# Kernel tuning notes

Hardware: AMD Instinct MI355X
Metric: run time of the kernel (lower is better)

Reference implementation:

```python
import jax, jax.numpy as jnp
import numpy as np

N = 50000      # nodes
E = 800000     # edges (avg degree 16)
IN = 256       # in_feat
OUT = 256      # out_feat
R = 8          # num_rels
B = 4          # num_bases
EPS = 1e-5
NEG_SLOPE = 0.1


def setup_inputs() -> dict:
    key = jax.random.key(0)
    ks = jax.random.split(key, 10)
    node_feats = jax.random.normal(ks[0], (N, IN), dtype=jnp.float32)
    src = jax.random.randint(ks[1], (E,), 0, N, dtype=jnp.int32)
    dst = jax.random.randint(ks[2], (E,), 0, N, dtype=jnp.int32)
    edge_types = jax.random.randint(ks[3], (E,), 0, R, dtype=jnp.int32)
    # RGCN basis-decomposition parameters
    bases = jax.random.normal(ks[4], (B, IN, OUT), dtype=jnp.float32) * (1.0 / np.sqrt(IN))
    comp = jax.random.normal(ks[5], (R, B), dtype=jnp.float32) * (1.0 / np.sqrt(B))
    loop_weight = jax.random.normal(ks[6], (IN, OUT), dtype=jnp.float32) * (1.0 / np.sqrt(IN))
    bias = jnp.zeros((OUT,), dtype=jnp.float32)
    gamma = jnp.ones((OUT,), dtype=jnp.float32)
    beta = jnp.zeros((OUT,), dtype=jnp.float32)
    return {"node_feats": node_feats, "src": src, "dst": dst, "edge_types": edge_types,
            "bases": bases, "comp": comp, "loop_weight": loop_weight, "bias": bias,
            "gamma": gamma, "beta": beta}


def reference(node_feats, src, dst, edge_types, bases, comp, loop_weight, bias, gamma, beta):
    # Basis decomposition: W_r = sum_b comp[r,b] * V_b  -> [R, IN, OUT]
    W = jnp.einsum('rb,bio->rio', comp, bases)
    # Transform all node features under every relation once (avoids per-edge [E,IN,OUT] gather)
    transformed = jnp.einsum('ni,rio->rno', node_feats, W)   # [R, N, OUT]
    msg = transformed[edge_types, src]                        # [E, OUT] gather per edge
    agg = jax.ops.segment_sum(msg, dst, num_segments=N)      # scatter-add to destinations
    # DGL RelGraphConv defaults: self-loop transform + bias
    h = agg + node_feats @ loop_weight + bias                 # [N, OUT]
    # LeakyReLU(0.1)
    h = jnp.where(h > 0, h, NEG_SLOPE * h)
    # LayerNorm over feature dim
    mu = jnp.mean(h, axis=-1, keepdims=True)
    var = jnp.mean(jnp.square(h - mu), axis=-1, keepdims=True)
    return gamma * (h - mu) * jax.lax.rsqrt(var + EPS) + beta
```

## Files before the change

kernel.cpp:

```cpp
#include <hip/hip_runtime.h>

#define NN 50000
#define MP 50048
#define EE 800000
#define RCOLS 2304

typedef __attribute__((ext_vector_type(8))) short short8;
typedef __attribute__((ext_vector_type(4))) float f32x4;

__device__ __forceinline__ float bf2f(unsigned short u) {
  unsigned int x = ((unsigned int)u) << 16;
  float f; __builtin_memcpy(&f, &x, 4); return f;
}
__device__ __forceinline__ unsigned short f2bf(float f) {
  unsigned int x; __builtin_memcpy(&x, &f, 4);
  return (unsigned short)((x + 0x7fffu + ((x >> 16) & 1u)) >> 16);
}

constexpr size_t OFF_XB   = 0;
constexpr size_t OFF_WT   = 25624576;
constexpr size_t OFF_T    = 26804224;
constexpr size_t OFF_CNT  = 257425408;
constexpr size_t OFF_OFFS = 257625408;
constexpr size_t OFF_CUR  = 257825412;
constexpr size_t OFF_EIX  = 258025412;

__global__ __launch_bounds__(256) void build_w_kernel(
    const float* __restrict__ bases, const float* __restrict__ comp,
    const float* __restrict__ loopw, unsigned short* __restrict__ WT) {
  int idx = blockIdx.x * 256 + threadIdx.x;
  if (idx >= RCOLS * 256) return;
  int ogl = idx >> 8;
  int i   = idx & 255;
  float v;
  if (ogl < 2048) {
    int r = ogl >> 8, o = ogl & 255;
    v = 0.f;
#pragma unroll
    for (int b = 0; b < 4; ++b)
      v += comp[r * 4 + b] * bases[((size_t)b * 256 + i) * 256 + o];
  } else {
    v = loopw[i * 256 + (ogl & 255)];
  }
  WT[idx] = f2bf(v);
}

__global__ __launch_bounds__(256) void convert_x_kernel(
    const float* __restrict__ X, unsigned short* __restrict__ Xb) {
  size_t e0 = ((size_t)blockIdx.x * 256 + threadIdx.x) * 4;
  if (e0 >= (size_t)MP * 256) return;
  float4 v = make_float4(0.f, 0.f, 0.f, 0.f);
  if (e0 < (size_t)NN * 256) v = *(const float4*)(X + e0);
  ushort4 o;
  o.x = f2bf(v.x); o.y = f2bf(v.y); o.z = f2bf(v.z); o.w = f2bf(v.w);
  *(ushort4*)(Xb + e0) = o;
}

__global__ __launch_bounds__(256) void gemm_kernel(
    const unsigned short* __restrict__ A,
    const unsigned short* __restrict__ Bt,
    unsigned short* __restrict__ C) {
  __shared__ __align__(16) unsigned short As[128 * 64];
  __shared__ __align__(16) unsigned short Bs[128 * 64];
  const int tid  = threadIdx.x;
  const int lane = tid & 63;
  const int wave = tid >> 6;
  const int wm = wave >> 1, wn = wave & 1;
  const int m0 = blockIdx.x * 128;
  const int n0 = blockIdx.y * 128;

  f32x4 acc[4][4] = {};

  const int srow = tid >> 3;
  const int ke   = (tid & 7) * 8;
  const unsigned int ldsbase = (unsigned int)((tid & ~63) * 16);

  for (int k0 = 0; k0 < 256; k0 += 64) {
#pragma unroll
    for (int p = 0; p < 4; ++p) {
      int row = p * 32 + srow;
      const unsigned short* ga = A  + (size_t)(m0 + row) * 256 + k0 + ke;
      const unsigned short* gb = Bt + (size_t)(n0 + row) * 256 + k0 + ke;
      unsigned int lo = p * 4096 + ldsbase;
      __builtin_amdgcn_global_load_lds(
          (const __attribute__((address_space(1))) unsigned int*)ga,
          (__attribute__((address_space(3))) unsigned int*)((char*)As + lo), 16, 0, 0);
      __builtin_amdgcn_global_load_lds(
          (const __attribute__((address_space(1))) unsigned int*)gb,
          (__attribute__((address_space(3))) unsigned int*)((char*)Bs + lo), 16, 0, 0);
    }
    __syncthreads();

    const int rfr = lane & 15;
    const int kgr = (lane >> 4) * 8;
#pragma unroll
    for (int kk = 0; kk < 2; ++kk) {
      short8 af[4], bfr[4];
#pragma unroll
      for (int m = 0; m < 4; ++m)
        af[m] = *(const short8*)&As[(wm * 64 + m * 16 + rfr) * 64 + kk * 32 + kgr];
#pragma unroll
      for (int n = 0; n < 4; ++n)
        bfr[n] = *(const short8*)&Bs[(wn * 64 + n * 16 + rfr) * 64 + kk * 32 + kgr];
#pragma unroll
      for (int m = 0; m < 4; ++m)
#pragma unroll
        for (int n = 0; n < 4; ++n)
          acc[m][n] = __builtin_amdgcn_mfma_f32_16x16x32_bf16(af[m], bfr[n], acc[m][n], 0, 0, 0);
    }
    __syncthreads();
  }

  const int orow = (lane >> 4) * 4;
  const int ocol = lane & 15;
#pragma unroll
  for (int m = 0; m < 4; ++m)
#pragma unroll
    for (int n = 0; n < 4; ++n) {
      int gr = m0 + wm * 64 + m * 16 + orow;
      int gc = n0 + wn * 64 + n * 16 + ocol;
      unsigned short* cp = C + (size_t)gr * RCOLS + gc;
#pragma unroll
      for (int j = 0; j < 4; ++j)
        cp[(size_t)j * RCOLS] = f2bf(acc[m][n][j]);
    }
}

__global__ __launch_bounds__(256) void count_kernel(const int* __restrict__ dst,
                                                    int* __restrict__ counts) {
  int e = blockIdx.x * 256 + threadIdx.x;
  if (e < EE) atomicAdd(&counts[dst[e]], 1);
}

__global__ __launch_bounds__(1024) void scan_kernel(const int* __restrict__ counts,
                                                    int* __restrict__ offsets) {
  __shared__ int wsum[16];
  __shared__ int carry_s;
  int tid = threadIdx.x, lane = tid & 63, wid = tid >> 6;
  if (tid == 0) carry_s = 0;
  __syncthreads();
  for (int base = 0; base < NN; base += 1024) {
    int i = base + tid;
    int v = (i < NN) ? counts[i] : 0;
    int incl = v;
#pragma unroll
    for (int d = 1; d < 64; d <<= 1) {
      int t = __shfl_up(incl, d, 64);
      if (lane >= d) incl += t;
    }
    if (lane == 63) wsum[wid] = incl;
    __syncthreads();
    int wpre = 0;
    for (int w = 0; w < wid; ++w) wpre += wsum[w];
    if (i < NN) offsets[i] = carry_s + wpre + incl - v;
    __syncthreads();
    if (tid == 1023) carry_s += wpre + incl;
    __syncthreads();
  }
  if (threadIdx.x == 0) offsets[NN] = carry_s;
}

__global__ __launch_bounds__(256) void scatter_kernel(
    const int* __restrict__ src, const int* __restrict__ dst,
    const int* __restrict__ etype, const int* __restrict__ offsets,
    int* __restrict__ cursor, unsigned int* __restrict__ eoff) {
  int e = blockIdx.x * 256 + threadIdx.x;
  if (e < EE) {
    int d = dst[e];
    int pos = atomicAdd(&cursor[d], 1);
    eoff[offsets[d] + pos] = (unsigned int)(src[e] * RCOLS + etype[e] * 256);
  }
}

__global__ __launch_bounds__(256) void finalize_kernel(
    const unsigned short* __restrict__ T, const int* __restrict__ offsets,
    const unsigned int* __restrict__ eoff,
    const float* __restrict__ bias, const float* __restrict__ gamma,
    const float* __restrict__ beta, float* __restrict__ out) {
  int wid = threadIdx.x >> 6, lane = threadIdx.x & 63;
  int n = blockIdx.x * 4 + wid;
  int o4 = lane * 4;
  float a0 = 0.f, a1 = 0.f, a2 = 0.f, a3 = 0.f;
  int s = offsets[n], e = offsets[n + 1];
  for (int i = s; i < e; ++i) {
    ushort4 v = *(const ushort4*)(T + (size_t)eoff[i] + o4);
    a0 += bf2f(v.x); a1 += bf2f(v.y); a2 += bf2f(v.z); a3 += bf2f(v.w);
  }
  ushort4 sl = *(const ushort4*)(T + (size_t)n * RCOLS + 2048 + o4);
  float4 bi = *(const float4*)(bias + o4);
  a0 += bf2f(sl.x) + bi.x; a1 += bf2f(sl.y) + bi.y;
  a2 += bf2f(sl.z) + bi.z; a3 += bf2f(sl.w) + bi.w;
  a0 = a0 > 0.f ? a0 : 0.1f * a0;
  a1 = a1 > 0.f ? a1 : 0.1f * a1;
  a2 = a2 > 0.f ? a2 : 0.1f * a2;
  a3 = a3 > 0.f ? a3 : 0.1f * a3;
  float sum = a0 + a1 + a2 + a3;
  float sq  = a0 * a0 + a1 * a1 + a2 * a2 + a3 * a3;
#pragma unroll
  for (int m = 32; m >= 1; m >>= 1) {
    sum += __shfl_xor(sum, m);
    sq  += __shfl_xor(sq, m);
  }
  float mu  = sum * (1.f / 256.f);
  float var = sq * (1.f / 256.f) - mu * mu;
  float inv = rsqrtf(var + 1e-5f);
  float4 g = *(const float4*)(gamma + o4);
  float4 be = *(const float4*)(beta + o4);
  float4 o;
  o.x = g.x * (a0 - mu) * inv + be.x;
  o.y = g.y * (a1 - mu) * inv + be.y;
  o.z = g.z * (a2 - mu) * inv + be.z;
  o.w = g.w * (a3 - mu) * inv + be.w;
  *(float4*)(out + (size_t)n * 256 + o4) = o;
}

extern "C" void kernel_launch(void* const* d_in, const int* in_sizes, int n_in,
                              void* d_out, int out_size, void* d_ws, size_t ws_size,
                              hipStream_t stream) {
  const float* node_feats = (const float*)d_in[0];
  const int*   src        = (const int*)d_in[1];
  const int*   dst        = (const int*)d_in[2];
  const int*   etype      = (const int*)d_in[3];
  const float* bases      = (const float*)d_in[4];
  const float* comp       = (const float*)d_in[5];
  const float* loopw      = (const float*)d_in[6];
  const float* bias       = (const float*)d_in[7];
  const float* gamma      = (const float*)d_in[8];
  const float* beta       = (const float*)d_in[9];
  float* out = (float*)d_out;

  char* ws = (char*)d_ws;
  unsigned short* Xb   = (unsigned short*)(ws + OFF_XB);
  unsigned short* WT   = (unsigned short*)(ws + OFF_WT);
  unsigned short* T    = (unsigned short*)(ws + OFF_T);
  int*            cnts = (int*)(ws + OFF_CNT);
  int*            offs = (int*)(ws + OFF_OFFS);
  int*            cur  = (int*)(ws + OFF_CUR);
  unsigned int*   eoff = (unsigned int*)(ws + OFF_EIX);

  build_w_kernel<<<(RCOLS * 256 + 255) / 256, 256, 0, stream>>>(bases, comp, loopw, WT);
  convert_x_kernel<<<((MP * 256 / 4) + 255) / 256, 256, 0, stream>>>(node_feats, Xb);
  gemm_kernel<<<dim3(MP / 128, RCOLS / 128), 256, 0, stream>>>(Xb, WT, T);

  hipMemsetAsync(cnts, 0, NN * 4, stream);
  hipMemsetAsync(cur, 0, NN * 4, stream);
  count_kernel<<<(EE + 255) / 256, 256, 0, stream>>>(dst, cnts);
  scan_kernel<<<1, 1024, 0, stream>>>(cnts, offs);
  scatter_kernel<<<(EE + 255) / 256, 256, 0, stream>>>(src, dst, etype, offs, cur, eoff);

  finalize_kernel<<<NN / 4, 256, 0, stream>>>(T, offs, eoff, bias, gamma, beta, out);
}
```

Baseline: 499.3 us.

## Aggregate features per relation before transform and fuse GEMM with LayerNorm epilogue

Reorders the computation so edges first gather bf16 node features into per-relation sums (plus a self-loop slot), producing an N x 2304 matrix. A single K=2304 GEMM then projects it to 256 outputs, with bias, LeakyReLU and LayerNorm fused into the epilogue. This removes the large N x 2304 transformed-feature write and its random per-edge reads, plus the separate finalize kernel. In exchange it writes and reads an equally large aggregate buffer, uses a register-heavy switch-based accumulator in the gather, and rounds aggregated sums to bf16 before the matmul.

```diff
diff --git a/kernel.cpp b/kernel.cpp
--- a/kernel.cpp
+++ b/kernel.cpp
@@ -3,7 +3,7 @@
 #define NN 50000
 #define MP 50048
 #define EE 800000
-#define RCOLS 2304
+#define KK 2304
 
 typedef __attribute__((ext_vector_type(8))) short short8;
 typedef __attribute__((ext_vector_type(4))) float f32x4;
@@ -18,112 +18,38 @@
 }
 
 constexpr size_t OFF_XB   = 0;
-constexpr size_t OFF_WT   = 25624576;
-constexpr size_t OFF_T    = 26804224;
-constexpr size_t OFF_CNT  = 257425408;
-constexpr size_t OFF_OFFS = 257625408;
-constexpr size_t OFF_CUR  = 257825412;
-constexpr size_t OFF_EIX  = 258025412;
+constexpr size_t OFF_WT   = 25600000;
+constexpr size_t OFF_G    = 26779648;
+constexpr size_t OFF_CNT  = 257400832;
+constexpr size_t OFF_OFFS = 257600832;
+constexpr size_t OFF_CUR  = 257800836;
+constexpr size_t OFF_EIX  = 258000836;
 
 __global__ __launch_bounds__(256) void build_w_kernel(
     const float* __restrict__ bases, const float* __restrict__ comp,
-    const float* __restrict__ loopw, unsigned short* __restrict__ WT) {
-  int idx = blockIdx.x * 256 + threadIdx.x;
-  if (idx >= RCOLS * 256) return;
-  int ogl = idx >> 8;
-  int i   = idx & 255;
+    const float* __restrict__ loopw, unsigned short* __restrict__ Bt) {
+  int kg = blockIdx.x * 256 + threadIdx.x;
+  int o  = blockIdx.y;
   float v;
-  if (ogl < 2048) {
-    int r = ogl >> 8, o = ogl & 255;
+  if (kg < 2048) {
+    int r = kg >> 8, i = kg & 255;
     v = 0.f;
 #pragma unroll
     for (int b = 0; b < 4; ++b)
       v += comp[r * 4 + b] * bases[((size_t)b * 256 + i) * 256 + o];
   } else {
-    v = loopw[i * 256 + (ogl & 255)];
-  }
-  WT[idx] = f2bf(v);
+    v = loopw[(kg & 255) * 256 + o];
+  }
+  Bt[(size_t)o * KK + kg] = f2bf(v);
 }
 
 __global__ __launch_bounds__(256) void convert_x_kernel(
     const float* __restrict__ X, unsigned short* __restrict__ Xb) {
   size_t e0 = ((size_t)blockIdx.x * 256 + threadIdx.x) * 4;
-  if (e0 >= (size_t)MP * 256) return;
-  float4 v = make_float4(0.f, 0.f, 0.f, 0.f);
-  if (e0 < (size_t)NN * 256) v = *(const float4*)(X + e0);
+  float4 v = *(const float4*)(X + e0);
   ushort4 o;
   o.x = f2bf(v.x); o.y = f2bf(v.y); o.z = f2bf(v.z); o.w = f2bf(v.w);
   *(ushort4*)(Xb + e0) = o;
-}
-
-__global__ __launch_bounds__(256) void gemm_kernel(
-    const unsigned short* __restrict__ A,
-    const unsigned short* __restrict__ Bt,
-    unsigned short* __restrict__ C) {
-  __shared__ __align__(16) unsigned short As[128 * 64];
-  __shared__ __align__(16) unsigned short Bs[128 * 64];
-  const int tid  = threadIdx.x;
-  const int lane = tid & 63;
-  const int wave = tid >> 6;
-  const int wm = wave >> 1, wn = wave & 1;
-  const int m0 = blockIdx.x * 128;
-  const int n0 = blockIdx.y * 128;
-
-  f32x4 acc[4][4] = {};
-
-  const int srow = tid >> 3;
-  const int ke   = (tid & 7) * 8;
-  const unsigned int ldsbase = (unsigned int)((tid & ~63) * 16);
-
-  for (int k0 = 0; k0 < 256; k0 += 64) {
-#pragma unroll
-    for (int p = 0; p < 4; ++p) {
-      int row = p * 32 + srow;
-      const unsigned short* ga = A  + (size_t)(m0 + row) * 256 + k0 + ke;
-      const unsigned short* gb = Bt + (size_t)(n0 + row) * 256 + k0 + ke;
-      unsigned int lo = p * 4096 + ldsbase;
-      __builtin_amdgcn_global_load_lds(
-          (const __attribute__((address_space(1))) unsigned int*)ga,
-          (__attribute__((address_space(3))) unsigned int*)((char*)As + lo), 16, 0, 0);
-      __builtin_amdgcn_global_load_lds(
-          (const __attribute__((address_space(1))) unsigned int*)gb,
-          (__attribute__((address_space(3))) unsigned int*)((char*)Bs + lo), 16, 0, 0);
-    }
-    __syncthreads();
-
-    const int rfr = lane & 15;
-    const int kgr = (lane >> 4) * 8;
-#pragma unroll
-    for (int kk = 0; kk < 2; ++kk) {
-      short8 af[4], bfr[4];
-#pragma unroll
-      for (int m = 0; m < 4; ++m)
-        af[m] = *(const short8*)&As[(wm * 64 + m * 16 + rfr) * 64 + kk * 32 + kgr];
-#pragma unroll
-      for (int n = 0; n < 4; ++n)
-        bfr[n] = *(const short8*)&Bs[(wn * 64 + n * 16 + rfr) * 64 + kk * 32 + kgr];
-#pragma unroll
-      for (int m = 0; m < 4; ++m)
-#pragma unroll
-        for (int n = 0; n < 4; ++n)
-          acc[m][n] = __builtin_amdgcn_mfma_f32_16x16x32_bf16(af[m], bfr[n], acc[m][n], 0, 0, 0);
-    }
-    __syncthreads();
-  }
-
-  const int orow = (lane >> 4) * 4;
-  const int ocol = lane & 15;
-#pragma unroll
-  for (int m = 0; m < 4; ++m)
-#pragma unroll
-    for (int n = 0; n < 4; ++n) {
-      int gr = m0 + wm * 64 + m * 16 + orow;
-      int gc = n0 + wn * 64 + n * 16 + ocol;
-      unsigned short* cp = C + (size_t)gr * RCOLS + gc;
-#pragma unroll
-      for (int j = 0; j < 4; ++j)
-        cp[(size_t)j * RCOLS] = f2bf(acc[m][n][j]);
-    }
 }
 
 __global__ __launch_bounds__(256) void count_kernel(const int* __restrict__ dst,
@@ -168,50 +94,167 @@
   if (e < EE) {
     int d = dst[e];
     int pos = atomicAdd(&cursor[d], 1);
-    eoff[offsets[d] + pos] = (unsigned int)(src[e] * RCOLS + etype[e] * 256);
-  }
-}
-
-__global__ __launch_bounds__(256) void finalize_kernel(
-    const unsigned short* __restrict__ T, const int* __restrict__ offsets,
-    const unsigned int* __restrict__ eoff,
+    eoff[offsets[d] + pos] = ((unsigned int)src[e] << 3) | (unsigned int)etype[e];
+  }
+}
+
+#define ACCUM(PK, V)                                                              \
+  { float f0 = bf2f((V).x), f1 = bf2f((V).y), f2 = bf2f((V).z), f3 = bf2f((V).w); \
+    switch ((PK) & 7u) {                                                          \
+      case 0: acc[0][0]+=f0; acc[0][1]+=f1; acc[0][2]+=f2; acc[0][3]+=f3; break;  \
+      case 1: acc[1][0]+=f0; acc[1][1]+=f1; acc[1][2]+=f2; acc[1][3]+=f3; break;  \
+      case 2: acc[2][0]+=f0; acc[2][1]+=f1; acc[2][2]+=f2; acc[2][3]+=f3; break;  \
+      case 3: acc[3][0]+=f0; acc[3][1]+=f1; acc[3][2]+=f2; acc[3][3]+=f3; break;  \
+      case 4: acc[4][0]+=f0; acc[4][1]+=f1; acc[4][2]+=f2; acc[4][3]+=f3; break;  \
+      case 5: acc[5][0]+=f0; acc[5][1]+=f1; acc[5][2]+=f2; acc[5][3]+=f3; break;  \
+      case 6: acc[6][0]+=f0; acc[6][1]+=f1; acc[6][2]+=f2; acc[6][3]+=f3; break;  \
+      default:acc[7][0]+=f0; acc[7][1]+=f1; acc[7][2]+=f2; acc[7][3]+=f3; break;  \
+    } }
+
+__global__ __launch_bounds__(256) void gather_kernel(
+    const unsigned short* __restrict__ Xb, const int* __restrict__ offsets,
+    const unsigned int* __restrict__ eoff, unsigned short* __restrict__ G) {
+  int wid = threadIdx.x >> 6, lane = threadIdx.x & 63;
+  int d = blockIdx.x * 4 + wid;
+  int o4 = lane * 4;
+  unsigned short* gp = G + (size_t)d * KK + o4;
+  if (d >= NN) {
+    ushort4 z = {0, 0, 0, 0};
+#pragma unroll
+    for (int r = 0; r < 9; ++r) *(ushort4*)(gp + r * 256) = z;
+    return;
+  }
+  float acc[8][4] = {};
+  int s = offsets[d], e = offsets[d + 1];
+  int i = s;
+  for (; i + 1 < e; i += 2) {
+    unsigned int pk0 = eoff[i], pk1 = eoff[i + 1];
+    ushort4 v0 = *(const ushort4*)(Xb + (size_t)(pk0 >> 3) * 256 + o4);
+    ushort4 v1 = *(const ushort4*)(Xb + (size_t)(pk1 >> 3) * 256 + o4);
+    ACCUM(pk0, v0)
+    ACCUM(pk1, v1)
+  }
+  if (i < e) {
+    unsigned int pk = eoff[i];
+    ushort4 v = *(const ushort4*)(Xb + (size_t)(pk >> 3) * 256 + o4);
+    ACCUM(pk, v)
+  }
+#pragma unroll
+  for (int r = 0; r < 8; ++r) {
+    ushort4 o;
+    o.x = f2bf(acc[r][0]); o.y = f2bf(acc[r][1]);
+    o.z = f2bf(acc[r][2]); o.w = f2bf(acc[r][3]);
+    *(ushort4*)(gp + r * 256) = o;
+  }
+  *(ushort4*)(gp + 2048) = *(const ushort4*)(Xb + (size_t)d * 256 + o4);
+}
+
+__global__ __launch_bounds__(512) void gemm_fused_kernel(
+    const unsigned short* __restrict__ G, const unsigned short* __restrict__ Bt,
     const float* __restrict__ bias, const float* __restrict__ gamma,
     const float* __restrict__ beta, float* __restrict__ out) {
-  int wid = threadIdx.x >> 6, lane = threadIdx.x & 63;
-  int n = blockIdx.x * 4 + wid;
-  int o4 = lane * 4;
-  float a0 = 0.f, a1 = 0.f, a2 = 0.f, a3 = 0.f;
-  int s = offsets[n], e = offsets[n + 1];
-  for (int i = s; i < e; ++i) {
-    ushort4 v = *(const ushort4*)(T + (size_t)eoff[i] + o4);
-    a0 += bf2f(v.x); a1 += bf2f(v.y); a2 += bf2f(v.z); a3 += bf2f(v.w);
-  }
-  ushort4 sl = *(const ushort4*)(T + (size_t)n * RCOLS + 2048 + o4);
-  float4 bi = *(const float4*)(bias + o4);
-  a0 += bf2f(sl.x) + bi.x; a1 += bf2f(sl.y) + bi.y;
-  a2 += bf2f(sl.z) + bi.z; a3 += bf2f(sl.w) + bi.w;
-  a0 = a0 > 0.f ? a0 : 0.1f * a0;
-  a1 = a1 > 0.f ? a1 : 0.1f * a1;
-  a2 = a2 > 0.f ? a2 : 0.1f * a2;
-  a3 = a3 > 0.f ? a3 : 0.1f * a3;
-  float sum = a0 + a1 + a2 + a3;
-  float sq  = a0 * a0 + a1 * a1 + a2 * a2 + a3 * a3;
-#pragma unroll
-  for (int m = 32; m >= 1; m >>= 1) {
-    sum += __shfl_xor(sum, m);
-    sq  += __shfl_xor(sq, m);
-  }
-  float mu  = sum * (1.f / 256.f);
-  float var = sq * (1.f / 256.f) - mu * mu;
-  float inv = rsqrtf(var + 1e-5f);
-  float4 g = *(const float4*)(gamma + o4);
-  float4 be = *(const float4*)(beta + o4);
-  float4 o;
-  o.x = g.x * (a0 - mu) * inv + be.x;
-  o.y = g.y * (a1 - mu) * inv + be.y;
-  o.z = g.z * (a2 - mu) * inv + be.z;
-  o.w = g.w * (a3 - mu) * inv + be.w;
-  *(float4*)(out + (size_t)n * 256 + o4) = o;
+  __shared__ __align__(16) unsigned short As[64 * 64];
+  __shared__ __align__(16) unsigned short Bs[256 * 64];
+  __shared__ float psum[64][4], psq[64][4];
+  __shared__ float smu[64], sinv[64];
+  const int tid = threadIdx.x, lane = tid & 63, wave = tid >> 6;
+  const int wm = wave >> 2, wn = wave & 3;
+  const int m0 = blockIdx.x * 64;
+
+  f32x4 acc[2][4] = {};
+  const int arow = tid >> 3;
+  const int ke   = (tid & 7) * 8;
+  const unsigned int wbase = (unsigned int)((tid & ~63) * 16);
+
+  for (int k0 = 0; k0 < KK; k0 += 64) {
+    {
+      const unsigned short* ga = G + (size_t)(m0 + arow) * KK + k0 + ke;
+      __builtin_amdgcn_global_load_lds(
+          (const __attribute__((address_space(1))) unsigned int*)ga,
+          (__attribute__((address_space(3))) unsigned int*)((char*)As + wbase), 16, 0, 0);
+    }
+#pragma unroll
+    for (int p = 0; p < 4; ++p) {
+      const unsigned short* gb = Bt + (size_t)(p * 64 + arow) * KK + k0 + ke;
+      __builtin_amdgcn_global_load_lds(
+          (const __attribute__((address_space(1))) unsigned int*)gb,
+          (__attribute__((address_space(3))) unsigned int*)((char*)Bs + p * 8192 + wbase), 16, 0, 0);
+    }
+    __syncthreads();
+
+    const int rfr = lane & 15;
+    const int kgr = (lane >> 4) * 8;
+#pragma unroll
+    for (int kk = 0; kk < 2; ++kk) {
+      short8 af[2], bfv[4];
+#pragma unroll
+      for (int m = 0; m < 2; ++m)
+        af[m] = *(const short8*)&As[(wm * 32 + m * 16 + rfr) * 64 + kk * 32 + kgr];
+#pragma unroll
+      for (int n = 0; n < 4; ++n)
+        bfv[n] = *(const short8*)&Bs[(wn * 64 + n * 16 + rfr) * 64 + kk * 32 + kgr];
+#pragma unroll
+      for (int m = 0; m < 2; ++m)
+#pragma unroll
+        for (int n = 0; n < 4; ++n)
+          acc[m][n] = __builtin_amdgcn_mfma_f32_16x16x32_bf16(af[m], bfv[n], acc[m][n], 0, 0, 0);
+    }
+    __syncthreads();
+  }
+
+  const int q = lane >> 4, c = lane & 15;
+  int cols[4]; float bv[4], gv[4], bev[4];
+#pragma unroll
+  for (int n = 0; n < 4; ++n) {
+    cols[n] = wn * 64 + n * 16 + c;
+    bv[n] = bias[cols[n]]; gv[n] = gamma[cols[n]]; bev[n] = beta[cols[n]];
+  }
+#pragma unroll
+  for (int m = 0; m < 2; ++m)
+#pragma unroll
+    for (int n = 0; n < 4; ++n)
+#pragma unroll
+      for (int j = 0; j < 4; ++j) {
+        float h = acc[m][n][j] + bv[n];
+        acc[m][n][j] = h > 0.f ? h : 0.1f * h;
+      }
+#pragma unroll
+  for (int m = 0; m < 2; ++m)
+#pragma unroll
+    for (int j = 0; j < 4; ++j) {
+      float s = 0.f, ss = 0.f;
+#pragma unroll
+      for (int n = 0; n < 4; ++n) { float h = acc[m][n][j]; s += h; ss += h * h; }
+#pragma unroll
+      for (int mask = 1; mask < 16; mask <<= 1) {
+        s  += __shfl_xor(s, mask);
+        ss += __shfl_xor(ss, mask);
+      }
+      int rl = wm * 32 + m * 16 + q * 4 + j;
+      if (c == 0) { psum[rl][wn] = s; psq[rl][wn] = ss; }
+    }
+  __syncthreads();
+  if (tid < 64) {
+    float s  = psum[tid][0] + psum[tid][1] + psum[tid][2] + psum[tid][3];
+    float ss = psq[tid][0] + psq[tid][1] + psq[tid][2] + psq[tid][3];
+    float mu = s * (1.f / 256.f);
+    float var = ss * (1.f / 256.f) - mu * mu;
+    smu[tid] = mu; sinv[tid] = rsqrtf(var + 1e-5f);
+  }
+  __syncthreads();
+#pragma unroll
+  for (int m = 0; m < 2; ++m)
+#pragma unroll
+    for (int j = 0; j < 4; ++j) {
+      int rl = wm * 32 + m * 16 + q * 4 + j;
+      int gr = m0 + rl;
+      if (gr < NN) {
+        float mu = smu[rl], inv = sinv[rl];
+#pragma unroll
+        for (int n = 0; n < 4; ++n)
+          out[(size_t)gr * 256 + cols[n]] = gv[n] * (acc[m][n][j] - mu) * inv + bev[n];
+      }
+    }
 }
 
 extern "C" void kernel_launch(void* const* d_in, const int* in_sizes, int n_in,
@@ -232,15 +275,14 @@
   char* ws = (char*)d_ws;
   unsigned short* Xb   = (unsigned short*)(ws + OFF_XB);
   unsigned short* WT   = (unsigned short*)(ws + OFF_WT);
-  unsigned short* T    = (unsigned short*)(ws + OFF_T);
+  unsigned short* G    = (unsigned short*)(ws + OFF_G);
   int*            cnts = (int*)(ws + OFF_CNT);
   int*            offs = (int*)(ws + OFF_OFFS);
   int*            cur  = (int*)(ws + OFF_CUR);
   unsigned int*   eoff = (unsigned int*)(ws + OFF_EIX);
 
-  build_w_kernel<<<(RCOLS * 256 + 255) / 256, 256, 0, stream>>>(bases, comp, loopw, WT);
-  convert_x_kernel<<<((MP * 256 / 4) + 255) / 256, 256, 0, stream>>>(node_feats, Xb);
-  gemm_kernel<<<dim3(MP / 128, RCOLS / 128), 256, 0, stream>>>(Xb, WT, T);
+  build_w_kernel<<<dim3(9, 256), 256, 0, stream>>>(bases, comp, loopw, WT);
+  convert_x_kernel<<<NN * 256 / 4 / 256, 256, 0, stream>>>(node_feats, Xb);
 
   hipMemsetAsync(cnts, 0, NN * 4, stream);
   hipMemsetAsync(cur, 0, NN * 4, stream);
@@ -248,5 +290,6 @@
   scan_kernel<<<1, 1024, 0, stream>>>(cnts, offs);
   scatter_kernel<<<(EE + 255) / 256, 256, 0, stream>>>(src, dst, etype, offs, cur, eoff);
 
-  finalize_kernel<<<NN / 4, 256, 0, stream>>>(T, offs, eoff, bias, gamma, beta, out);
-}
+  gather_kernel<<<MP / 4, 256, 0, stream>>>(Xb, offs, eoff, G);
+  gemm_fused_kernel<<<MP / 64, 512, 0, stream>>>(G, WT, bias, gamma, beta, out);
+}
```

Result: slower. 942.0 us (+88.7%).
